# Kernel tuning notes

Measured on AMD Instinct MI355X. Metric: run time of the kernel, lower is better.

## Reference

```python
import jax, jax.numpy as jnp
import numpy as np

N = 50000
E = 500000
H = 128


def _linear(x, w, b):
    # torch nn.Linear: y = x @ W.T + b, W is [out, in]
    return x @ w.T + b


def _layer(x, h, edge_index, w0_w, w0_b, wl_w, wl_b, w1_w, w1_b):
    # PyG MessagePassing(aggr='add', flow='target_to_source'):
    # x_j = h[edge_index[1]], scatter-add into edge_index[0], dim_size = N
    msg = h[edge_index[1]]                               # [E, H] gather
    aggr = jax.ops.segment_sum(msg, edge_index[0], num_segments=h.shape[0])  # [N, H]
    return _linear(aggr, wl_w, wl_b) + _linear(h, w0_w, w0_b) + _linear(x, w1_w, w1_b)


def setup_inputs() -> dict:
    key = jax.random.key(0)
    ks = jax.random.split(key, 12)
    wscale = 0.05
    return {
        "x_a": jax.random.normal(ks[0], (N, H), jnp.float32),
        "x_b": jax.random.normal(ks[1], (N, H), jnp.float32),
        "edge_ab": jax.random.randint(ks[2], (2, E), 0, N, jnp.int32),
        "edge_ba": jax.random.randint(ks[3], (2, E), 0, N, jnp.int32),
        "conv0_w0_w": jax.random.normal(ks[4], (H, H), jnp.float32) * wscale,
        "conv0_w0_b": jnp.zeros((H,), jnp.float32),
        "conv0_wl_w": jax.random.normal(ks[5], (H, H), jnp.float32) * wscale,
        "conv0_wl_b": jnp.zeros((H,), jnp.float32),
        "conv0_w1_w": jax.random.normal(ks[6], (H, H), jnp.float32) * wscale,
        "conv0_w1_b": jnp.zeros((H,), jnp.float32),
        "conv1_w0_w": jax.random.normal(ks[7], (H, H), jnp.float32) * wscale,
        "conv1_w0_b": jnp.zeros((H,), jnp.float32),
        "conv1_wl_w": jax.random.normal(ks[8], (H, H), jnp.float32) * wscale,
        "conv1_wl_b": jnp.zeros((H,), jnp.float32),
        "conv1_w1_w": jax.random.normal(ks[9], (H, H), jnp.float32) * wscale,
        "conv1_w1_b": jnp.zeros((H,), jnp.float32),
        "out_w": jax.random.normal(ks[10], (H, H), jnp.float32) * wscale,
        "out_b": jnp.zeros((H,), jnp.float32),
    }


def reference(x_a, x_b, edge_ab, edge_ba,
              conv0_w0_w, conv0_w0_b, conv0_wl_w, conv0_wl_b, conv0_w1_w, conv0_w1_b,
              conv1_w0_w, conv1_w0_b, conv1_wl_w, conv1_wl_b, conv1_w1_w, conv1_w1_b,
              out_w, out_b):
    # metapath = [(a, r1, b), (b, r2, a)], loop over reversed(metapath):
    # iter 0: conv_idx=1, edge (b, r2, a), dst='a'
    h_a = jax.nn.relu(_layer(x_a, x_a, edge_ba,
                             conv1_w0_w, conv1_w0_b, conv1_wl_w, conv1_wl_b, conv1_w1_w, conv1_w1_b))
    # iter 1: conv_idx=0, edge (a, r1, b), dst='b'
    h_b = jax.nn.relu(_layer(x_b, x_b, edge_ab,
                             conv0_w0_w, conv0_w0_b, conv0_wl_w, conv0_wl_b, conv0_w1_w, conv0_w1_b))
    # start_type = 'a'
    return _linear(h_a, out_w, out_b)
```

## Files before the change

kernel.cpp:

```cpp
#include <hip/hip_runtime.h>
#include <hip/hip_bf16.h>

#define NN 50000
#define NE 500000
#define HD 128
#define SCAN_B ((NN + 255) / 256)
#define PREP_B 24
#define PREPX_B 3125
#define SETUP_B (PREP_B + PREPX_B + SCAN_B)

typedef __bf16 bf16;
typedef __attribute__((ext_vector_type(8))) __bf16 bf16x8;
typedef __attribute__((ext_vector_type(4))) float floatx4;

__device__ inline float u2f(unsigned int lo16) {
    union { unsigned int i; float f; } c; c.i = lo16 << 16; return c.f;
}

__device__ inline bf16x8 cvt8(floatx4 a, floatx4 b) {
    bf16x8 r;
#pragma unroll
    for (int j = 0; j < 4; j++) { r[j] = (bf16)a[j]; r[j + 4] = (bf16)b[j]; }
    return r;
}

__device__ inline void split8(const floatx4 f0, const floatx4 f1, bf16x8& hi, bf16x8& lo) {
#pragma unroll
    for (int j = 0; j < 4; j++) {
        float a = f0[j]; bf16 h = (bf16)a; hi[j] = h; lo[j] = (bf16)(a - (float)h);
        float b = f1[j]; bf16 g = (bf16)b; hi[j + 4] = g; lo[j + 4] = (bf16)(b - (float)g);
    }
}

__device__ inline bf16x8 zero8() {
    bf16x8 v;
#pragma unroll
    for (int j = 0; j < 8; j++) v[j] = (bf16)0.f;
    return v;
}

__global__ __launch_bounds__(256) void k_setup(
    const float* __restrict__ wl, const float* __restrict__ w0, const float* __restrict__ w1,
    const float* __restrict__ bl, const float* __restrict__ b0, const float* __restrict__ b1,
    const float* __restrict__ ow, const float* __restrict__ ob,
    const float* __restrict__ x,
    bf16* __restrict__ wlb, bf16* __restrict__ w01b, bf16* __restrict__ owb,
    float* __restrict__ bias1, float* __restrict__ bias2,
    bf16* __restrict__ xb, int* __restrict__ dcur,
    int tier)
{
    const int b = blockIdx.x, tid = threadIdx.x;
    if (b < PREP_B) {
        int g = b * 256 + tid;
        int m = g >> 11, off = (g & 2047) << 3;
        if (m == 0) {
            const floatx4 a = *(const floatx4*)(wl + off);
            const floatx4 c = *(const floatx4*)(wl + off + 4);
            *(bf16x8*)(wlb + off) = cvt8(a, c);
        } else if (m == 1) {
            floatx4 a = *(const floatx4*)(w0 + off);
            floatx4 c = *(const floatx4*)(w0 + off + 4);
            const floatx4 d = *(const floatx4*)(w1 + off);
            const floatx4 e = *(const floatx4*)(w1 + off + 4);
#pragma unroll
            for (int j = 0; j < 4; j++) { a[j] += d[j]; c[j] += e[j]; }
            *(bf16x8*)(w01b + off) = cvt8(a, c);
        } else {
            const floatx4 a = *(const floatx4*)(ow + off);
            const floatx4 c = *(const floatx4*)(ow + off + 4);
            *(bf16x8*)(owb + off) = cvt8(a, c);
        }
        if (g < 128) bias1[g] = bl[g] + b0[g] + b1[g];
        else if (g < 256) bias2[g - 128] = ob[g - 128];
    } else if (b < PREP_B + PREPX_B) {
        if (tier >= 2) {
            int off = ((b - PREP_B) * 256 + tid) << 3;
            const floatx4 a = *(const floatx4*)(x + off);
            const floatx4 c = *(const floatx4*)(x + off + 4);
            *(bf16x8*)(xb + off) = cvt8(a, c);
        }
    } else {
        if (tier >= 1) {
            int i = (b - PREP_B - PREPX_B) * 256 + tid;
            if (i < NN) dcur[i] = 0;
        }
    }
}

__global__ __launch_bounds__(256) void k_hist(const int* __restrict__ edge,
                                              int* __restrict__ cnt) {
    int e = blockIdx.x * 256 + threadIdx.x;
    if (e < NE) atomicAdd(&cnt[edge[e]], 1);
}

__global__ __launch_bounds__(256) void k_scan1(const int* __restrict__ cnt,
                                               int* __restrict__ excl,
                                               int* __restrict__ bsum) {
    __shared__ int s[256];
    const int t = threadIdx.x, i = blockIdx.x * 256 + t;
    int c = (i < NN) ? cnt[i] : 0;
    s[t] = c; __syncthreads();
    int v = c;
    for (int off = 1; off < 256; off <<= 1) {
        int u = (t >= off) ? s[t - off] : 0;
        __syncthreads();
        v += u; s[t] = v;
        __syncthreads();
    }
    if (i < NN) excl[i] = v - c;
    if (t == 255) bsum[blockIdx.x] = v;
}

__global__ __launch_bounds__(256) void k_scan23(int* __restrict__ offs,
                                                const int* __restrict__ bsum,
                                                int* __restrict__ cur) {
    __shared__ int s[256];
    const int t = threadIdx.x;
    int c = (t < SCAN_B) ? bsum[t] : 0;
    s[t] = c; __syncthreads();
    int v = c;
    for (int off = 1; off < 256; off <<= 1) {
        int u = (t >= off) ? s[t - off] : 0;
        __syncthreads();
        v += u; s[t] = v;
        __syncthreads();
    }
    const int bpre = (blockIdx.x > 0) ? s[blockIdx.x - 1] : 0;
    int i = blockIdx.x * 256 + t;
    if (i < NN) {
        int o = offs[i] + bpre;
        offs[i] = o;
        cur[i] = o;
    } else if (i == NN) {
        offs[NN] = NE;
    }
}

__global__ __launch_bounds__(256) void k_fill(const int* __restrict__ edge,
                                              int* __restrict__ cur,
                                              int* __restrict__ csr_src) {
    int e = blockIdx.x * 256 + threadIdx.x;
    if (e < NE) {
        int dst = edge[e];
        int src = edge[NE + e];
        int pos = atomicAdd(&cur[dst], 1);
        csr_src[pos] = src;
    }
}

__global__ __launch_bounds__(256) void k_aggr_b(const unsigned int* __restrict__ xb2,
                                                const int* __restrict__ offs,
                                                const int* __restrict__ csr_src,
                                                float* __restrict__ aggr) {
    int w = (blockIdx.x * 256 + threadIdx.x) >> 6;
    int lane = threadIdx.x & 63;
    if (w >= NN) return;
    int s = offs[w], e = offs[w + 1];
    float ax = 0.f, ay = 0.f;
    int d = s;
    for (; d + 3 < e; d += 4) {
        int s0 = csr_src[d], s1 = csr_src[d + 1], s2 = csr_src[d + 2], s3 = csr_src[d + 3];
        unsigned int v0 = xb2[s0 * 64 + lane];
        unsigned int v1 = xb2[s1 * 64 + lane];
        unsigned int v2 = xb2[s2 * 64 + lane];
        unsigned int v3 = xb2[s3 * 64 + lane];
        ax += u2f(v0 & 0xffff) + u2f(v1 & 0xffff) + u2f(v2 & 0xffff) + u2f(v3 & 0xffff);
        ay += u2f(v0 >> 16) + u2f(v1 >> 16) + u2f(v2 >> 16) + u2f(v3 >> 16);
    }
    for (; d < e; d++) {
        unsigned int v = xb2[csr_src[d] * 64 + lane];
        ax += u2f(v & 0xffff); ay += u2f(v >> 16);
    }
    float2 o; o.x = ax; o.y = ay;
    ((float2*)aggr)[(size_t)w * 64 + lane] = o;
}

__global__ __launch_bounds__(256) void k_aggr_f(const float* __restrict__ x,
                                                const int* __restrict__ offs,
                                                const int* __restrict__ csr_src,
                                                float* __restrict__ aggr) {
    int w = (blockIdx.x * 256 + threadIdx.x) >> 6;
    int lane = threadIdx.x & 63;
    if (w >= NN) return;
    int s = offs[w], e = offs[w + 1];
    const float2* xp = (const float2*)x;
    float ax = 0.f, ay = 0.f;
    int d = s;
    for (; d + 1 < e; d += 2) {
        int s0 = csr_src[d], s1 = csr_src[d + 1];
        float2 v0 = xp[(size_t)s0 * 64 + lane];
        float2 v1 = xp[(size_t)s1 * 64 + lane];
        ax += v0.x + v1.x; ay += v0.y + v1.y;
    }
    if (d < e) {
        float2 v = xp[(size_t)csr_src[d] * 64 + lane];
        ax += v.x; ay += v.y;
    }
    float2 o; o.x = ax; o.y = ay;
    ((float2*)aggr)[(size_t)w * 64 + lane] = o;
}

__global__ __launch_bounds__(256) void k_zero(float* __restrict__ p) {
    int i = blockIdx.x * 256 + threadIdx.x;
    floatx4 z = {0.f, 0.f, 0.f, 0.f};
    ((floatx4*)p)[i] = z;
}

__global__ __launch_bounds__(256) void k_scatter(const float* __restrict__ x,
                                                 const int* __restrict__ edge,
                                                 float* __restrict__ aggr) {
    int tid = blockIdx.x * 256 + threadIdx.x;
    int e = tid >> 5;
    int c = (tid & 31) << 2;
    int dst = edge[e];
    int src = edge[NE + e];
    const floatx4 v = *(const floatx4*)(x + src * HD + c);
    float* ap = aggr + dst * HD + c;
    unsafeAtomicAdd(ap + 0, v[0]);
    unsafeAtomicAdd(ap + 1, v[1]);
    unsafeAtomicAdd(ap + 2, v[2]);
    unsafeAtomicAdd(ap + 3, v[3]);
}

__global__ __launch_bounds__(256) void k_gemm12(
    const float* __restrict__ aggr, const float* __restrict__ x, const bf16* __restrict__ xb,
    int use_xb,
    const bf16* __restrict__ wlb, const bf16* __restrict__ w01b, const bf16* __restrict__ owb,
    const float* __restrict__ bias1, const float* __restrict__ bias2,
    float* __restrict__ out)
{
    __shared__ bf16 sA[128 * 136];
    __shared__ bf16 sB[128 * 136];
    __shared__ float b1_s[128], b2_s[128];
    float* tp = (float*)sB;
    const int tid = threadIdx.x;

#pragma unroll
    for (int it = 0; it < 8; it++) {
        int i = tid + it * 256;
        int r = i >> 4;
        int o = (i & 15) << 3;
        *(bf16x8*)(sA + r * 136 + o) = *(const bf16x8*)(wlb  + r * 128 + o);
        *(bf16x8*)(sB + r * 136 + o) = *(const bf16x8*)(w01b + r * 128 + o);
    }
    if (tid < 128) { b1_s[tid] = bias1[tid]; b2_s[tid] = bias2[tid]; }
    __syncthreads();

    const int lane = tid & 63;
    const int wv   = tid >> 6;
    const int ln   = lane & 15;
    const int quad = lane >> 4;
    const int row0 = blockIdx.x * 64 + wv * 16;
    const int arow = row0 + ln;
    const bool aok = arow < NN;

    floatx4 acc[8] = {};

#pragma unroll
    for (int kc = 0; kc < 4; kc++) {
        const int k0 = kc * 32 + quad * 8;
        bf16x8 a_hi = zero8(), a_lo = zero8(), a_x = zero8();
        if (aok) {
            const floatx4 f0 = *(const floatx4*)(aggr + arow * 128 + k0);
            const floatx4 f1 = *(const floatx4*)(aggr + arow * 128 + k0 + 4);
            split8(f0, f1, a_hi, a_lo);
            if (use_xb) {
                a_x = *(const bf16x8*)(xb + arow * 128 + k0);
            } else {
                const floatx4 g0 = *(const floatx4*)(x + arow * 128 + k0);
                const floatx4 g1 = *(const floatx4*)(x + arow * 128 + k0 + 4);
                a_x = cvt8(g0, g1);
            }
        }
#pragma unroll
        for (int nc = 0; nc < 8; nc++) {
            const bf16x8 bw  = *(const bf16x8*)(sA + (nc * 16 + ln) * 136 + k0);
            const bf16x8 bw2 = *(const bf16x8*)(sB + (nc * 16 + ln) * 136 + k0);
            acc[nc] = __builtin_amdgcn_mfma_f32_16x16x32_bf16(a_hi, bw,  acc[nc], 0, 0, 0);
            acc[nc] = __builtin_amdgcn_mfma_f32_16x16x32_bf16(a_lo, bw,  acc[nc], 0, 0, 0);
            acc[nc] = __builtin_amdgcn_mfma_f32_16x16x32_bf16(a_x,  bw2, acc[nc], 0, 0, 0);
        }
    }
    __syncthreads();

#pragma unroll
    for (int it = 0; it < 8; it++) {
        int i = tid + it * 256;
        int r = i >> 4;
        int o = (i & 15) << 3;
        *(bf16x8*)(sA + r * 136 + o) = *(const bf16x8*)(owb + r * 128 + o);
    }
#pragma unroll
    for (int nc = 0; nc < 8; nc++) {
        const int col = nc * 16 + ln;
        const float bv = b1_s[col];
#pragma unroll
        for (int r = 0; r < 4; r++) {
            float v = acc[nc][r] + bv;
            tp[wv * 2112 + (quad * 4 + r) * 132 + col] = (v > 0.f ? v : 0.f);
        }
        acc[nc][0] = acc[nc][1] = acc[nc][2] = acc[nc][3] = 0.f;
    }
    __syncthreads();

#pragma unroll
    for (int kc = 0; kc < 4; kc++) {
        const int k0 = kc * 32 + quad * 8;
        const floatx4 f0 = *(const floatx4*)(tp + wv * 2112 + ln * 132 + k0);
        const floatx4 f1 = *(const floatx4*)(tp + wv * 2112 + ln * 132 + k0 + 4);
        bf16x8 a_hi, a_lo;
        split8(f0, f1, a_hi, a_lo);
#pragma unroll
        for (int nc = 0; nc < 8; nc++) {
            const bf16x8 bw = *(const bf16x8*)(sA + (nc * 16 + ln) * 136 + k0);
            acc[nc] = __builtin_amdgcn_mfma_f32_16x16x32_bf16(a_hi, bw, acc[nc], 0, 0, 0);
            acc[nc] = __builtin_amdgcn_mfma_f32_16x16x32_bf16(a_lo, bw, acc[nc], 0, 0, 0);
        }
    }

#pragma unroll
    for (int nc = 0; nc < 8; nc++) {
        const int col = nc * 16 + ln;
        const float bv = b2_s[col];
#pragma unroll
        for (int r = 0; r < 4; r++) {
            const int row = row0 + quad * 4 + r;
            if (row < NN) out[row * 128 + col] = acc[nc][r] + bv;
        }
    }
}

extern "C" void kernel_launch(void* const* d_in, const int* in_sizes, int n_in,
                              void* d_out, int out_size, void* d_ws, size_t ws_size,
                              hipStream_t stream) {
    const float* x_a     = (const float*)d_in[0];
    const int*   edge_ba = (const int*)d_in[3];
    const float* c1_w0_w = (const float*)d_in[10];
    const float* c1_w0_b = (const float*)d_in[11];
    const float* c1_wl_w = (const float*)d_in[12];
    const float* c1_wl_b = (const float*)d_in[13];
    const float* c1_w1_w = (const float*)d_in[14];
    const float* c1_w1_b = (const float*)d_in[15];
    const float* out_w   = (const float*)d_in[16];
    const float* out_b   = (const float*)d_in[17];

    char* p = (char*)d_ws;
    float* aggr  = (float*)p;   p += (size_t)NN * HD * 4;
    bf16*  wlb   = (bf16*)p;    p += 32768;
    bf16*  w01b  = (bf16*)p;    p += 32768;
    bf16*  owb   = (bf16*)p;    p += 32768;
    float* bias1 = (float*)p;   p += 512;
    float* bias2 = (float*)p;   p += 512;
    const size_t WS_FALL = (size_t)(p - (char*)d_ws);
    int*   offs  = (int*)p;     p += 200064;
    int*   dcur  = (int*)p;     p += 200064;
    int*   csr   = (int*)p;     p += (size_t)NE * 4;
    int*   bsum  = (int*)p;     p += 1024;
    const size_t WS_CSR = (size_t)(p - (char*)d_ws);
    bf16*  xb    = (bf16*)p;    p += (size_t)NN * HD * 2;
    const size_t WS_FULL = (size_t)(p - (char*)d_ws);

    int tier = (ws_size >= WS_FULL) ? 2 : (ws_size >= WS_CSR) ? 1 : 0;

    k_setup<<<SETUP_B, 256, 0, stream>>>(c1_wl_w, c1_w0_w, c1_w1_w,
                                         c1_wl_b, c1_w0_b, c1_w1_b,
                                         out_w, out_b, x_a,
                                         wlb, w01b, owb, bias1, bias2,
                                         xb, dcur, tier);

    if (tier >= 1) {
        k_hist  <<<(NE + 255) / 256, 256, 0, stream>>>(edge_ba, dcur);
        k_scan1 <<<SCAN_B, 256, 0, stream>>>(dcur, offs, bsum);
        k_scan23<<<SCAN_B, 256, 0, stream>>>(offs, bsum, dcur);
        k_fill  <<<(NE + 255) / 256, 256, 0, stream>>>(edge_ba, dcur, csr);
        if (tier == 2) {
            k_aggr_b<<<(NN * 64 + 255) / 256, 256, 0, stream>>>((const unsigned int*)xb,
                                                                offs, csr, aggr);
        } else {
            k_aggr_f<<<(NN * 64 + 255) / 256, 256, 0, stream>>>(x_a, offs, csr, aggr);
        }
    } else {
        k_zero   <<<NN * HD / 4 / 256, 256, 0, stream>>>(aggr);
        k_scatter<<<NE * 32 / 256,     256, 0, stream>>>(x_a, edge_ba, aggr);
    }

    k_gemm12<<<(NN + 63) / 64, 256, 0, stream>>>(aggr, x_a, xb, (tier == 2) ? 1 : 0,
                                                 wlb, w01b, owb, bias1, bias2,
                                                 (float*)d_out);
}
```

Measured before the change: 225.0 us.

## Replace CSR build with fixed-capacity per-node buckets and atomic overflow

The histogram, two-level scan and CSR fill kernels are replaced by one fill pass that appends each source index into a fixed 128-slot bucket per destination node. Rare overflow edges are added directly into aggr with float atomics. Zeroing of aggr moves into the setup kernel. This removes three kernel launches and the scan dependency, at the cost of a much larger bucket workspace (NN*128 ints) and sparse, strided bucket reads during aggregation.

```diff
diff --git a/kernel.cpp b/kernel.cpp
--- a/kernel.cpp
+++ b/kernel.cpp
@@ -4,10 +4,12 @@
 #define NN 50000
 #define NE 500000
 #define HD 128
-#define SCAN_B ((NN + 255) / 256)
+#define CAP 128
 #define PREP_B 24
 #define PREPX_B 3125
-#define SETUP_B (PREP_B + PREPX_B + SCAN_B)
+#define ZAGGR_B 6250
+#define ZCUR_B ((NN + 255) / 256)
+#define SETUP_B (PREP_B + PREPX_B + ZAGGR_B + ZCUR_B)
 
 typedef __bf16 bf16;
 typedef __attribute__((ext_vector_type(8))) __bf16 bf16x8;
@@ -46,7 +48,7 @@
     const float* __restrict__ x,
     bf16* __restrict__ wlb, bf16* __restrict__ w01b, bf16* __restrict__ owb,
     float* __restrict__ bias1, float* __restrict__ bias2,
-    bf16* __restrict__ xb, int* __restrict__ dcur,
+    bf16* __restrict__ xb, float* __restrict__ aggr, int* __restrict__ cur,
     int tier)
 {
     const int b = blockIdx.x, tid = threadIdx.x;
@@ -73,93 +75,61 @@
         if (g < 128) bias1[g] = bl[g] + b0[g] + b1[g];
         else if (g < 256) bias2[g - 128] = ob[g - 128];
     } else if (b < PREP_B + PREPX_B) {
-        if (tier >= 2) {
+        if (tier >= 1) {
             int off = ((b - PREP_B) * 256 + tid) << 3;
             const floatx4 a = *(const floatx4*)(x + off);
             const floatx4 c = *(const floatx4*)(x + off + 4);
             *(bf16x8*)(xb + off) = cvt8(a, c);
         }
+    } else if (b < PREP_B + PREPX_B + ZAGGR_B) {
+        int i = (b - PREP_B - PREPX_B) * 256 + tid;
+        floatx4 z = {0.f, 0.f, 0.f, 0.f};
+        ((floatx4*)aggr)[i] = z;
     } else {
         if (tier >= 1) {
-            int i = (b - PREP_B - PREPX_B) * 256 + tid;
-            if (i < NN) dcur[i] = 0;
-        }
-    }
-}
-
-__global__ __launch_bounds__(256) void k_hist(const int* __restrict__ edge,
-                                              int* __restrict__ cnt) {
+            int i = (b - PREP_B - PREPX_B - ZAGGR_B) * 256 + tid;
+            if (i < NN) cur[i] = 0;
+        }
+    }
+}
+
+__global__ __launch_bounds__(256) void k_fillb(const int* __restrict__ edge,
+                                               const float* __restrict__ x,
+                                               int* __restrict__ cur,
+                                               int* __restrict__ bucket,
+                                               float* __restrict__ aggr) {
     int e = blockIdx.x * 256 + threadIdx.x;
-    if (e < NE) atomicAdd(&cnt[edge[e]], 1);
-}
-
-__global__ __launch_bounds__(256) void k_scan1(const int* __restrict__ cnt,
-                                               int* __restrict__ excl,
-                                               int* __restrict__ bsum) {
-    __shared__ int s[256];
-    const int t = threadIdx.x, i = blockIdx.x * 256 + t;
-    int c = (i < NN) ? cnt[i] : 0;
-    s[t] = c; __syncthreads();
-    int v = c;
-    for (int off = 1; off < 256; off <<= 1) {
-        int u = (t >= off) ? s[t - off] : 0;
-        __syncthreads();
-        v += u; s[t] = v;
-        __syncthreads();
-    }
-    if (i < NN) excl[i] = v - c;
-    if (t == 255) bsum[blockIdx.x] = v;
-}
-
-__global__ __launch_bounds__(256) void k_scan23(int* __restrict__ offs,
-                                                const int* __restrict__ bsum,
-                                                int* __restrict__ cur) {
-    __shared__ int s[256];
-    const int t = threadIdx.x;
-    int c = (t < SCAN_B) ? bsum[t] : 0;
-    s[t] = c; __syncthreads();
-    int v = c;
-    for (int off = 1; off < 256; off <<= 1) {
-        int u = (t >= off) ? s[t - off] : 0;
-        __syncthreads();
-        v += u; s[t] = v;
-        __syncthreads();
-    }
-    const int bpre = (blockIdx.x > 0) ? s[blockIdx.x - 1] : 0;
-    int i = blockIdx.x * 256 + t;
-    if (i < NN) {
-        int o = offs[i] + bpre;
-        offs[i] = o;
-        cur[i] = o;
-    } else if (i == NN) {
-        offs[NN] = NE;
-    }
-}
-
-__global__ __launch_bounds__(256) void k_fill(const int* __restrict__ edge,
-                                              int* __restrict__ cur,
-                                              int* __restrict__ csr_src) {
-    int e = blockIdx.x * 256 + threadIdx.x;
-    if (e < NE) {
-        int dst = edge[e];
-        int src = edge[NE + e];
-        int pos = atomicAdd(&cur[dst], 1);
-        csr_src[pos] = src;
-    }
-}
-
-__global__ __launch_bounds__(256) void k_aggr_b(const unsigned int* __restrict__ xb2,
-                                                const int* __restrict__ offs,
-                                                const int* __restrict__ csr_src,
-                                                float* __restrict__ aggr) {
+    if (e >= NE) return;
+    int dst = edge[e];
+    int src = edge[NE + e];
+    int pos = atomicAdd(&cur[dst], 1);
+    if (pos < CAP) {
+        bucket[dst * CAP + pos] = src;
+    } else {
+        const float* xr = x + (size_t)src * HD;
+        float* ar = aggr + (size_t)dst * HD;
+        for (int c = 0; c < HD; c++) unsafeAtomicAdd(ar + c, xr[c]);
+    }
+}
+
+__global__ __launch_bounds__(256) void k_aggr(const unsigned int* __restrict__ xb2,
+                                              const int* __restrict__ cur,
+                                              const int* __restrict__ bucket,
+                                              float* __restrict__ aggr) {
     int w = (blockIdx.x * 256 + threadIdx.x) >> 6;
     int lane = threadIdx.x & 63;
     if (w >= NN) return;
-    int s = offs[w], e = offs[w + 1];
+    int deg = cur[w];
+    int n = (deg < CAP) ? deg : CAP;
+    const int* bk = bucket + w * CAP;
     float ax = 0.f, ay = 0.f;
-    int d = s;
-    for (; d + 3 < e; d += 4) {
-        int s0 = csr_src[d], s1 = csr_src[d + 1], s2 = csr_src[d + 2], s3 = csr_src[d + 3];
+    if (deg > CAP) {
+        float2 init = ((float2*)aggr)[(size_t)w * 64 + lane];
+        ax = init.x; ay = init.y;
+    }
+    int d = 0;
+    for (; d + 3 < n; d += 4) {
+        int s0 = bk[d], s1 = bk[d + 1], s2 = bk[d + 2], s3 = bk[d + 3];
         unsigned int v0 = xb2[s0 * 64 + lane];
         unsigned int v1 = xb2[s1 * 64 + lane];
         unsigned int v2 = xb2[s2 * 64 + lane];
@@ -167,43 +137,12 @@
         ax += u2f(v0 & 0xffff) + u2f(v1 & 0xffff) + u2f(v2 & 0xffff) + u2f(v3 & 0xffff);
         ay += u2f(v0 >> 16) + u2f(v1 >> 16) + u2f(v2 >> 16) + u2f(v3 >> 16);
     }
-    for (; d < e; d++) {
-        unsigned int v = xb2[csr_src[d] * 64 + lane];
+    for (; d < n; d++) {
+        unsigned int v = xb2[bk[d] * 64 + lane];
         ax += u2f(v & 0xffff); ay += u2f(v >> 16);
     }
     float2 o; o.x = ax; o.y = ay;
     ((float2*)aggr)[(size_t)w * 64 + lane] = o;
-}
-
-__global__ __launch_bounds__(256) void k_aggr_f(const float* __restrict__ x,
-                                                const int* __restrict__ offs,
-                                                const int* __restrict__ csr_src,
-                                                float* __restrict__ aggr) {
-    int w = (blockIdx.x * 256 + threadIdx.x) >> 6;
-    int lane = threadIdx.x & 63;
-    if (w >= NN) return;
-    int s = offs[w], e = offs[w + 1];
-    const float2* xp = (const float2*)x;
-    float ax = 0.f, ay = 0.f;
-    int d = s;
-    for (; d + 1 < e; d += 2) {
-        int s0 = csr_src[d], s1 = csr_src[d + 1];
-        float2 v0 = xp[(size_t)s0 * 64 + lane];
-        float2 v1 = xp[(size_t)s1 * 64 + lane];
-        ax += v0.x + v1.x; ay += v0.y + v1.y;
-    }
-    if (d < e) {
-        float2 v = xp[(size_t)csr_src[d] * 64 + lane];
-        ax += v.x; ay += v.y;
-    }
-    float2 o; o.x = ax; o.y = ay;
-    ((float2*)aggr)[(size_t)w * 64 + lane] = o;
-}
-
-__global__ __launch_bounds__(256) void k_zero(float* __restrict__ p) {
-    int i = blockIdx.x * 256 + threadIdx.x;
-    floatx4 z = {0.f, 0.f, 0.f, 0.f};
-    ((floatx4*)p)[i] = z;
 }
 
 __global__ __launch_bounds__(256) void k_scatter(const float* __restrict__ x,
@@ -352,39 +291,28 @@
     float* bias1 = (float*)p;   p += 512;
     float* bias2 = (float*)p;   p += 512;
     const size_t WS_FALL = (size_t)(p - (char*)d_ws);
-    int*   offs  = (int*)p;     p += 200064;
-    int*   dcur  = (int*)p;     p += 200064;
-    int*   csr   = (int*)p;     p += (size_t)NE * 4;
-    int*   bsum  = (int*)p;     p += 1024;
-    const size_t WS_CSR = (size_t)(p - (char*)d_ws);
-    bf16*  xb    = (bf16*)p;    p += (size_t)NN * HD * 2;
-    const size_t WS_FULL = (size_t)(p - (char*)d_ws);
-
-    int tier = (ws_size >= WS_FULL) ? 2 : (ws_size >= WS_CSR) ? 1 : 0;
+    int*   cur    = (int*)p;    p += 200704;
+    int*   bucket = (int*)p;    p += (size_t)NN * CAP * 4;
+    bf16*  xb     = (bf16*)p;   p += (size_t)NN * HD * 2;
+    const size_t WS_BUCKET = (size_t)(p - (char*)d_ws);
+
+    const int tier = (ws_size >= WS_BUCKET) ? 1 : 0;
 
     k_setup<<<SETUP_B, 256, 0, stream>>>(c1_wl_w, c1_w0_w, c1_w1_w,
                                          c1_wl_b, c1_w0_b, c1_w1_b,
                                          out_w, out_b, x_a,
                                          wlb, w01b, owb, bias1, bias2,
-                                         xb, dcur, tier);
-
-    if (tier >= 1) {
-        k_hist  <<<(NE + 255) / 256, 256, 0, stream>>>(edge_ba, dcur);
-        k_scan1 <<<SCAN_B, 256, 0, stream>>>(dcur, offs, bsum);
-        k_scan23<<<SCAN_B, 256, 0, stream>>>(offs, bsum, dcur);
-        k_fill  <<<(NE + 255) / 256, 256, 0, stream>>>(edge_ba, dcur, csr);
-        if (tier == 2) {
-            k_aggr_b<<<(NN * 64 + 255) / 256, 256, 0, stream>>>((const unsigned int*)xb,
-                                                                offs, csr, aggr);
-        } else {
-            k_aggr_f<<<(NN * 64 + 255) / 256, 256, 0, stream>>>(x_a, offs, csr, aggr);
-        }
+                                         xb, aggr, cur, tier);
+
+    if (tier) {
+        k_fillb<<<(NE + 255) / 256, 256, 0, stream>>>(edge_ba, x_a, cur, bucket, aggr);
+        k_aggr <<<(NN * 64 + 255) / 256, 256, 0, stream>>>((const unsigned int*)xb,
+                                                           cur, bucket, aggr);
     } else {
-        k_zero   <<<NN * HD / 4 / 256, 256, 0, stream>>>(aggr);
-        k_scatter<<<NE * 32 / 256,     256, 0, stream>>>(x_a, edge_ba, aggr);
-    }
-
-    k_gemm12<<<(NN + 63) / 64, 256, 0, stream>>>(aggr, x_a, xb, (tier == 2) ? 1 : 0,
+        k_scatter<<<NE * 32 / 256, 256, 0, stream>>>(x_a, edge_ba, aggr);
+    }
+
+    k_gemm12<<<(NN + 63) / 64, 256, 0, stream>>>(aggr, x_a, xb, tier,
                                                  wlb, w01b, owb, bias1, bias2,
                                                  (float*)d_out);
 }
```

Result: faster. 200.9 us (-10.7%).
